# Kernel optimization log

Hardware: AMD Instinct MI355X
Metric: run time of the kernel (lower is better)

The kernel has to match this reference:

```python
import jax, jax.numpy as jnp
import numpy as np

B = 2; CIN = 64; COUT = 64; H = 192; W = 192
KH = 3; KW = 3; K = KH * KW; NC = 20
STRIDE = 1; PAD = 1; DIL = 1


def setup_inputs() -> dict:
    key = jax.random.key(0)
    ks = jax.random.split(key, 7)
    x = jax.random.normal(ks[0], (B, CIN, H, W), jnp.float32)
    input_LO = jax.random.uniform(ks[1], (B, NC, H, W), jnp.float32)
    output_LO = jax.random.uniform(ks[2], (B, NC, H, W), jnp.float32)  # HO=H, WO=W for k3 s1 p1
    weight = jax.random.normal(ks[3], (COUT, CIN, KH, KW), jnp.float32) * 0.05
    bias = jax.random.normal(ks[4], (COUT,), jnp.float32) * 0.05
    # conv_offset is zero-init in source; use small random weights so offsets are exercised
    off_w = jax.random.normal(ks[5], (2 * K, CIN, KH, KW), jnp.float32) * 0.01
    off_b = jnp.zeros((2 * K,), jnp.float32)
    return {"x": x, "input_LO": input_LO, "output_LO": output_LO,
            "weight": weight, "bias": bias, "off_w": off_w, "off_b": off_b}


def _gather(img_flat, idx):
    # img_flat: [B, C, H*W], idx: [B, N] -> [B, C, N]
    return jax.vmap(lambda im, ix: im[:, ix])(img_flat, idx)


def _bilinear(img, py, px, zero_pad):
    """Bilinear sample img [B,C,Hi,Wi] at pixel coords py/px [B,K,Ho,Wo].
    zero_pad=True -> zeros outside (deformable conv); False -> border clamp (grid_sample border)."""
    Bb, Cc, Hh, Ww = img.shape
    if not zero_pad:
        px = jnp.clip(px, 0.0, Ww - 1.0)
        py = jnp.clip(py, 0.0, Hh - 1.0)
    x0 = jnp.floor(px)
    y0 = jnp.floor(py)
    img_f = img.reshape(Bb, Cc, Hh * Ww)
    out = jnp.zeros((Bb, Cc) + px.shape[1:], img.dtype)
    for dy in (0.0, 1.0):
        for dx in (0.0, 1.0):
            yc = y0 + dy
            xc = x0 + dx
            w = (1.0 - jnp.abs(py - yc)) * (1.0 - jnp.abs(px - xc))
            if zero_pad:
                valid = (yc >= 0) & (yc <= Hh - 1) & (xc >= 0) & (xc <= Ww - 1)
                w = w * valid.astype(w.dtype)
            yi = jnp.clip(yc, 0, Hh - 1).astype(jnp.int32)
            xi = jnp.clip(xc, 0, Ww - 1).astype(jnp.int32)
            idx = (yi * Ww + xi).reshape(Bb, -1)
            g = _gather(img_f, idx).reshape((Bb, Cc) + px.shape[1:])
            out = out + g * w[:, None]
    return out


def reference(x, input_LO, output_LO, weight, bias, off_w, off_b):
    # 1) offset conv (torch chunk+cat is identity, so offset == conv_offset(x))
    offset = jax.lax.conv_general_dilated(
        x, off_w, (STRIDE, STRIDE), ((PAD, PAD), (PAD, PAD)),
        dimension_numbers=("NCHW", "OIHW", "NCHW")) + off_b[None, :, None, None]
    Bb, _, Ho, Wo = offset.shape
    off = offset.reshape(Bb, K, 2, Ho, Wo)
    off_y = off[:, :, 0]   # channel 2k   -> y offset
    off_x = off[:, :, 1]   # channel 2k+1 -> x offset
    hk = (jnp.arange(K) // KW).astype(x.dtype)[None, :, None, None]
    wk = (jnp.arange(K) % KW).astype(x.dtype)[None, :, None, None]

    # 2) mask: grid_sample label map at deformed locations (align_corners=True, border pad)
    hor = jnp.linspace(-1.0, 1.0, Wo)[None, None, None, :]
    ver = jnp.linspace(-1.0, 1.0, Ho)[None, None, :, None]
    gx = hor * STRIDE - PAD + (wk + off_x) / ((W - 1.0) / 2.0)
    gy = ver * STRIDE - PAD + (hk + off_y) / ((H - 1.0) / 2.0)
    px = (gx + 1.0) * (W - 1.0) / 2.0
    py = (gy + 1.0) * (H - 1.0) / 2.0
    samp_LO = _bilinear(input_LO, py, px, zero_pad=False)        # [B,NC,K,Ho,Wo]
    mask = jnp.einsum("bnkhw,bnhw->bkhw", samp_LO, output_LO)    # [B,K,Ho,Wo]

    # 3) modulated deformable conv (DCNv2 math, zero padding outside)
    base_y = (jnp.arange(Ho) * STRIDE - PAD).astype(x.dtype)[None, None, :, None]
    base_x = (jnp.arange(Wo) * STRIDE - PAD).astype(x.dtype)[None, None, None, :]
    py2 = base_y + hk * DIL + off_y
    px2 = base_x + wk * DIL + off_x
    samp = _bilinear(x, py2, px2, zero_pad=True)                 # [B,C,K,Ho,Wo]
    samp = samp * mask[:, None]
    out = jnp.einsum("bckhw,ock->bohw", samp, weight.reshape(COUT, CIN, K))
    return out + bias[None, :, None, None]
```

## Files before the change

kernel.cpp:

```cpp
#include <hip/hip_runtime.h>

#define Bn   2
#define CIN  64
#define COUT 64
#define Hd   192
#define Wd   192
#define HWd  (Hd*Wd)
#define Kk   9
#define NCh  20
#define NTILE 1152

typedef __attribute__((ext_vector_type(8))) short short8;
typedef __attribute__((ext_vector_type(4))) float f32x4;

static __device__ __forceinline__ ushort f2bf(float f) {
    unsigned u = __float_as_uint(f);
    u += 0x7fffu + ((u >> 16) & 1u);
    return (ushort)(u >> 16);
}
static __device__ __forceinline__ float bf2f(ushort v) {
    return __uint_as_float(((unsigned)v) << 16);
}

__global__ __launch_bounds__(256) void kT(const float* __restrict__ x,
        const float* __restrict__ inLO, const float* __restrict__ outLO,
        const float* __restrict__ w, const float* __restrict__ off_w,
        ushort* __restrict__ xtb, float* __restrict__ inLOt,
        float* __restrict__ outLOt, ushort* __restrict__ wtb,
        float* __restrict__ owt) {
    __shared__ float lds[20 * 257];
    int bid = blockIdx.x, tid = threadIdx.x;
    if (bid < 1152) {
        int b = bid / 576, p0 = (bid % 576) * 64;
        const float* src = x + b * CIN * HWd + p0;
        #pragma unroll
        for (int r = 0; r < 16; ++r) {
            int e = r * 256 + tid;
            int c = e >> 6, p = e & 63;
            lds[c * 65 + p] = src[c * HWd + p];
        }
        __syncthreads();
        ushort* dst = xtb + ((size_t)(b * HWd + p0)) * 64;
        #pragma unroll
        for (int r = 0; r < 16; ++r) {
            int e = r * 256 + tid;
            int p = e >> 6, c = e & 63;
            dst[e] = f2bf(lds[c * 65 + p]);
        }
    } else if (bid < 1728) {
        int q = bid - 1152;
        int t = q / 288; q %= 288;
        int b = q / 144, p0 = (q % 144) * 256;
        const float* src = (t == 0 ? inLO : outLO) + b * NCh * HWd + p0;
        float* dst = (t == 0 ? inLOt : outLOt) + b * NCh * HWd + p0 * NCh;
        #pragma unroll
        for (int r = 0; r < 20; ++r) {
            int e = r * 256 + tid;
            int n = e >> 8, p = e & 255;
            lds[n * 257 + p] = src[n * HWd + p];
        }
        __syncthreads();
        #pragma unroll
        for (int r = 0; r < 20; ++r) {
            int e = r * 256 + tid;
            int p = e / 20, n = e % 20;
            dst[e] = lds[n * 257 + p];
        }
    } else if (bid < 1872) {
        int f = (bid - 1728) * 256 + tid;
        int e = f & 7, lane = (f >> 3) & 63;
        int kt = (f >> 9) & 1, nt = (f >> 10) & 3, tap = f >> 12;
        int o = nt * 16 + (lane & 15);
        int c = kt * 32 + (lane >> 4) * 8 + e;
        wtb[f] = f2bf(w[(o * CIN + c) * Kk + tap]);
    } else {
        int idx = (bid - 1872) * 256 + tid;
        if (idx < 18 * 576) {
            int oc = idx % 18, ct = idx / 18;
            int c = ct / 9, tap = ct % 9;
            owt[idx] = off_w[(oc * CIN + c) * Kk + tap];
        }
    }
}

__global__ __launch_bounds__(256) void k1_offset_conv(const float* __restrict__ x,
        const float* __restrict__ owt, const float* __restrict__ off_b,
        float* __restrict__ off) {
    int tid = threadIdx.x;
    int half = blockIdx.x & 1;
    int oc0 = half * 9;
    int pix = (blockIdx.x >> 1) * 256 + tid;
    int b = pix / HWd, pp = pix % HWd;
    int jj = pp % Wd, ii = pp / Wd;
    float acc[9];
    #pragma unroll
    for (int q = 0; q < 9; ++q) acc[q] = off_b[oc0 + q];
    const float* xb = x + b * CIN * HWd;
    for (int c = 0; c < CIN; ++c) {
        const float* xc = xb + c * HWd;
        float v[9];
        #pragma unroll
        for (int dy = 0; dy < 3; ++dy) {
            int yy = ii + dy - 1;
            bool vy = (yy >= 0 && yy < Hd);
            #pragma unroll
            for (int dx = 0; dx < 3; ++dx) {
                int xx = jj + dx - 1;
                bool ok = vy && (xx >= 0) && (xx < Wd);
                int yc = min(max(yy, 0), Hd - 1);
                int xc2 = min(max(xx, 0), Wd - 1);
                float t = xc[yc * Wd + xc2];
                v[dy * 3 + dx] = ok ? t : 0.f;
            }
        }
        const float* wrow = owt + c * 9 * 18 + oc0;
        #pragma unroll
        for (int tap = 0; tap < 9; ++tap) {
            #pragma unroll
            for (int q = 0; q < 9; ++q)
                acc[q] += v[tap] * wrow[tap * 18 + q];
        }
    }
    float* op = off + b * 18 * HWd + pp;
    #pragma unroll
    for (int q = 0; q < 9; ++q) op[(oc0 + q) * HWd] = acc[q];
}

__global__ __launch_bounds__(256) void k2_mask(const float* __restrict__ inLOt,
        const float* __restrict__ outLOt, const float* __restrict__ off,
        float* __restrict__ mask) {
    int t = blockIdx.x * 256 + threadIdx.x;
    int p = t % HWd;
    int k = (t / HWd) % Kk;
    int b = t / (Kk * HWd);
    int j = p % Wd, i = p / Wd;
    float offy = off[(b * 18 + 2 * k) * HWd + p];
    float offx = off[(b * 18 + 2 * k + 1) * HWd + p];
    float py = (float)(i + (k / 3)) + offy - 95.5f;
    float px = (float)(j + (k % 3)) + offx - 95.5f;
    py = fminf(fmaxf(py, 0.f), 191.f);
    px = fminf(fmaxf(px, 0.f), 191.f);
    float y0f = floorf(py), x0f = floorf(px);
    float ly = py - y0f, lx = px - x0f;
    int y0 = (int)y0f, x0 = (int)x0f;
    int y1 = min(y0 + 1, Hd - 1), x1 = min(x0 + 1, Wd - 1);
    float w00 = (1.f - ly) * (1.f - lx);
    float w01 = (1.f - ly) * lx;
    float w10 = ly * (1.f - lx);
    float w11 = ly * lx;
    const float4* L00 = (const float4*)(inLOt + (b * HWd + y0 * Wd + x0) * NCh);
    const float4* L01 = (const float4*)(inLOt + (b * HWd + y0 * Wd + x1) * NCh);
    const float4* L10 = (const float4*)(inLOt + (b * HWd + y1 * Wd + x0) * NCh);
    const float4* L11 = (const float4*)(inLOt + (b * HWd + y1 * Wd + x1) * NCh);
    const float4* O   = (const float4*)(outLOt + (b * HWd + p) * NCh);
    float acc = 0.f;
    #pragma unroll
    for (int n = 0; n < 5; ++n) {
        float4 a = L00[n], bb = L01[n], c = L10[n], d = L11[n], o = O[n];
        acc += (w00 * a.x + w01 * bb.x + w10 * c.x + w11 * d.x) * o.x;
        acc += (w00 * a.y + w01 * bb.y + w10 * c.y + w11 * d.y) * o.y;
        acc += (w00 * a.z + w01 * bb.z + w10 * c.z + w11 * d.z) * o.z;
        acc += (w00 * a.w + w01 * bb.w + w10 * c.w + w11 * d.w) * o.w;
    }
    mask[(b * Kk + k) * HWd + p] = acc;
}

__global__ __launch_bounds__(256) void k3_part(const ushort* __restrict__ xtb,
        const float* __restrict__ off, const float* __restrict__ mask,
        const ushort* __restrict__ wtb, float* __restrict__ part) {
    __shared__ __align__(16) ushort A_lds[4 * 2 * 64 * 8];
    int tid = threadIdx.x;
    int bid = blockIdx.x;
    int h = bid >= NTILE;
    int tb = bid - (h ? NTILE : 0);
    int t0 = h ? 5 : 0, t1 = h ? 9 : 5;
    int jt = tb % 3, i = (tb / 3) % Hd, b = tb / (3 * Hd);
    int j0 = jt * 64;

    int lane = tid & 63;
    int wv_id = tid >> 6;
    int wm = wv_id >> 1;
    int wn = wv_id & 1;

    int pxo = lane & 7;
    int chunk = lane >> 3;
    int kt_s = chunk >> 2;
    int ksub = chunk & 3;
    const ushort* xb = xtb + (size_t)b * HWd * 64;

    f32x4 acc[2][2];
    #pragma unroll
    for (int mi = 0; mi < 2; ++mi)
        #pragma unroll
        for (int ni = 0; ni < 2; ++ni)
            acc[mi][ni] = (f32x4){0.f, 0.f, 0.f, 0.f};

    for (int t = t0; t < t1; ++t) {
        short8 bf[2][2];
        #pragma unroll
        for (int kt = 0; kt < 2; ++kt)
            #pragma unroll
            for (int ni = 0; ni < 2; ++ni) {
                int nt = wn * 2 + ni;
                bf[kt][ni] = *(const short8*)(wtb +
                    ((((t * 4 + nt) * 2 + kt) * 64 + lane) << 3));
            }

        #pragma unroll
        for (int r = 0; r < 2; ++r) {
            int px_loc = (wv_id << 4) + (r << 3) + pxo;
            int pix = i * Wd + j0 + px_loc;
            float offy = off[(b * 18 + 2 * t) * HWd + pix];
            float offx = off[(b * 18 + 2 * t + 1) * HWd + pix];
            float m = mask[(b * Kk + t) * HWd + pix];
            float py = (float)(i - 1 + (t / 3)) + offy;
            float px = (float)(j0 + px_loc - 1 + (t % 3)) + offx;
            float y0f = floorf(py), x0f = floorf(px);
            float ly = py - y0f, lx = px - x0f;
            int y0 = (int)y0f, x0 = (int)x0f;
            int y1 = y0 + 1, x1 = x0 + 1;
            bool vy0 = (y0 >= 0 && y0 < Hd), vy1 = (y1 >= 0 && y1 < Hd);
            bool vx0 = (x0 >= 0 && x0 < Wd), vx1 = (x1 >= 0 && x1 < Wd);
            float w00 = (vy0 && vx0) ? (1.f - ly) * (1.f - lx) * m : 0.f;
            float w01 = (vy0 && vx1) ? (1.f - ly) * lx * m : 0.f;
            float w10 = (vy1 && vx0) ? ly * (1.f - lx) * m : 0.f;
            float w11 = (vy1 && vx1) ? ly * lx * m : 0.f;
            int y0c = min(max(y0, 0), Hd - 1), y1c = min(max(y1, 0), Hd - 1);
            int x0c = min(max(x0, 0), Wd - 1), x1c = min(max(x1, 0), Wd - 1);
            const short8* g0p = (const short8*)(xb + (size_t)(y0c * Wd + x0c) * 64 + chunk * 8);
            const short8* g1p = (const short8*)(xb + (size_t)(y0c * Wd + x1c) * 64 + chunk * 8);
            const short8* g2p = (const short8*)(xb + (size_t)(y1c * Wd + x0c) * 64 + chunk * 8);
            const short8* g3p = (const short8*)(xb + (size_t)(y1c * Wd + x1c) * 64 + chunk * 8);
            short8 g0 = *g0p, g1 = *g1p, g2 = *g2p, g3 = *g3p;
            short8 pk;
            #pragma unroll
            for (int e = 0; e < 8; ++e) {
                float s = w00 * bf2f((ushort)g0[e]) + w01 * bf2f((ushort)g1[e])
                        + w10 * bf2f((ushort)g2[e]) + w11 * bf2f((ushort)g3[e]);
                pk[e] = (short)f2bf(s);
            }
            *(short8*)&A_lds[(((wv_id * 2 + kt_s) * 64 + ksub * 16 +
                               ((r << 3) + pxo)) << 3)] = pk;
        }
        __syncthreads();

        #pragma unroll
        for (int kt = 0; kt < 2; ++kt) {
            #pragma unroll
            for (int mi = 0; mi < 2; ++mi) {
                int mt2 = wm * 2 + mi;
                short8 af = *(const short8*)&A_lds[(((mt2 * 2 + kt) * 64 + lane) << 3)];
                acc[mi][0] = __builtin_amdgcn_mfma_f32_16x16x32_bf16(
                                 af, bf[kt][0], acc[mi][0], 0, 0, 0);
                acc[mi][1] = __builtin_amdgcn_mfma_f32_16x16x32_bf16(
                                 af, bf[kt][1], acc[mi][1], 0, 0, 0);
            }
        }
        __syncthreads();
    }

    float* pb = part + ((size_t)(h * NTILE + tb) << 12);
    int colo = lane & 15;
    int rb = (lane >> 4) * 4;
    #pragma unroll
    for (int ni = 0; ni < 2; ++ni) {
        int o = wn * 32 + ni * 16 + colo;
        #pragma unroll
        for (int mi = 0; mi < 2; ++mi) {
            int p0 = wm * 32 + mi * 16 + rb;
            float4 r;
            r.x = acc[mi][ni][0];
            r.y = acc[mi][ni][1];
            r.z = acc[mi][ni][2];
            r.w = acc[mi][ni][3];
            *(float4*)(pb + o * 64 + p0) = r;
        }
    }
}

__global__ __launch_bounds__(256) void k4_reduce(const float* __restrict__ part,
        const float* __restrict__ bias, float* __restrict__ out) {
    int e4 = blockIdx.x * 256 + threadIdx.x;
    int tile = e4 >> 10;
    int wi = e4 & 1023;
    int o = wi >> 4;
    int p0 = (wi & 15) << 2;
    const float4* pp = (const float4*)part;
    float4 a = pp[e4];
    float4 c = pp[e4 + NTILE * 1024];
    float bv = bias[o];
    int jt = tile % 3, i = (tile / 3) % Hd, b = tile / (3 * Hd);
    float4 r;
    r.x = a.x + c.x + bv;
    r.y = a.y + c.y + bv;
    r.z = a.z + c.z + bv;
    r.w = a.w + c.w + bv;
    *(float4*)(out + ((size_t)(b * COUT + o) * HWd) + i * Wd + jt * 64 + p0) = r;
}

extern "C" void kernel_launch(void* const* d_in, const int* in_sizes, int n_in,
                              void* d_out, int out_size, void* d_ws, size_t ws_size,
                              hipStream_t stream) {
    const float* x      = (const float*)d_in[0];
    const float* inLO   = (const float*)d_in[1];
    const float* outLO  = (const float*)d_in[2];
    const float* weight = (const float*)d_in[3];
    const float* bias   = (const float*)d_in[4];
    const float* off_w  = (const float*)d_in[5];
    const float* off_b  = (const float*)d_in[6];
    float* out = (float*)d_out;

    float*  off    = (float*)d_ws;
    float*  mask   = off    + Bn * 18 * HWd;
    ushort* wtb    = (ushort*)(mask + Bn * Kk * HWd);
    float*  owt    = (float*)(mask + Bn * Kk * HWd) + Kk * CIN * COUT;
    ushort* xtb    = (ushort*)(owt + 576 * 18);
    float*  inLOt  = (float*)(xtb + (size_t)Bn * HWd * CIN);
    float*  outLOt = inLOt  + (size_t)Bn * HWd * NCh;
    float*  part   = outLOt + (size_t)Bn * HWd * NCh;

    kT<<<1913, 256, 0, stream>>>(x, inLO, outLO, weight, off_w,
                                 xtb, inLOt, outLOt, wtb, owt);
    k1_offset_conv<<<576, 256, 0, stream>>>(x, owt, off_b, off);
    k2_mask<<<2592, 256, 0, stream>>>(inLOt, outLOt, off, mask);
    k3_part<<<2 * NTILE, 256, 0, stream>>>(xtb, off, mask, wtb, part);
    k4_reduce<<<4608, 256, 0, stream>>>(part, bias, out);
}
```

Measured before the change: 209.2 us.

## Compute offset conv with bf16 MFMA and store label maps as padded bf16

The scalar fp32 offset convolution is replaced by an implicit-GEMM kernel that reads the channel-last bf16 copy of x and accumulates with 16x16x32 bf16 MFMA instructions. Offset weights are pre-packed into the MFMA B-fragment layout, with output channels padded from 18 to 32. The input/output label maps are now transposed to bf16 with 20 channels padded to 24, so the mask kernel issues 16-byte loads and moves less data. The cost is lower precision in the offsets and the mask, and offsets feed the bilinear sample positions, so small rounding errors can shift sampling.

```diff
diff --git a/kernel.cpp b/kernel.cpp
--- a/kernel.cpp
+++ b/kernel.cpp
@@ -8,6 +8,7 @@
 #define HWd  (Hd*Wd)
 #define Kk   9
 #define NCh  20
+#define NCP  24
 #define NTILE 1152
 
 typedef __attribute__((ext_vector_type(8))) short short8;
@@ -25,9 +26,9 @@
 __global__ __launch_bounds__(256) void kT(const float* __restrict__ x,
         const float* __restrict__ inLO, const float* __restrict__ outLO,
         const float* __restrict__ w, const float* __restrict__ off_w,
-        ushort* __restrict__ xtb, float* __restrict__ inLOt,
-        float* __restrict__ outLOt, ushort* __restrict__ wtb,
-        float* __restrict__ owt) {
+        ushort* __restrict__ xtb, ushort* __restrict__ inLOb,
+        ushort* __restrict__ outLOb, ushort* __restrict__ wtb,
+        ushort* __restrict__ owtb) {
     __shared__ float lds[20 * 257];
     int bid = blockIdx.x, tid = threadIdx.x;
     if (bid < 1152) {
@@ -52,7 +53,7 @@
         int t = q / 288; q %= 288;
         int b = q / 144, p0 = (q % 144) * 256;
         const float* src = (t == 0 ? inLO : outLO) + b * NCh * HWd + p0;
-        float* dst = (t == 0 ? inLOt : outLOt) + b * NCh * HWd + p0 * NCh;
+        ushort* dst = (t == 0 ? inLOb : outLOb) + ((size_t)(b * HWd + p0)) * NCP;
         #pragma unroll
         for (int r = 0; r < 20; ++r) {
             int e = r * 256 + tid;
@@ -61,10 +62,10 @@
         }
         __syncthreads();
         #pragma unroll
-        for (int r = 0; r < 20; ++r) {
+        for (int r = 0; r < 24; ++r) {
             int e = r * 256 + tid;
-            int p = e / 20, n = e % 20;
-            dst[e] = lds[n * 257 + p];
+            int p = e / NCP, n = e - p * NCP;
+            dst[e] = (n < NCh) ? f2bf(lds[n * 257 + p]) : (ushort)0;
         }
     } else if (bid < 1872) {
         int f = (bid - 1728) * 256 + tid;
@@ -74,60 +75,72 @@
         int c = kt * 32 + (lane >> 4) * 8 + e;
         wtb[f] = f2bf(w[(o * CIN + c) * Kk + tap]);
     } else {
-        int idx = (bid - 1872) * 256 + tid;
-        if (idx < 18 * 576) {
-            int oc = idx % 18, ct = idx / 18;
-            int c = ct / 9, tap = ct % 9;
-            owt[idx] = off_w[(oc * CIN + c) * Kk + tap];
-        }
-    }
-}
-
-__global__ __launch_bounds__(256) void k1_offset_conv(const float* __restrict__ x,
-        const float* __restrict__ owt, const float* __restrict__ off_b,
+        int f = (bid - 1872) * 256 + tid;
+        if (f < 18432) {
+            int e = f & 7, lane = (f >> 3) & 63;
+            int kt = (f >> 9) & 1, nt = (f >> 10) & 1, tap = f >> 11;
+            int oc = nt * 16 + (lane & 15);
+            int c = kt * 32 + (lane >> 4) * 8 + e;
+            owtb[f] = (oc < 18) ? f2bf(off_w[(oc * CIN + c) * Kk + tap]) : (ushort)0;
+        }
+    }
+}
+
+__global__ __launch_bounds__(256) void k1_gemm(const ushort* __restrict__ xtb,
+        const ushort* __restrict__ owtb, const float* __restrict__ off_b,
         float* __restrict__ off) {
-    int tid = threadIdx.x;
-    int half = blockIdx.x & 1;
-    int oc0 = half * 9;
-    int pix = (blockIdx.x >> 1) * 256 + tid;
-    int b = pix / HWd, pp = pix % HWd;
-    int jj = pp % Wd, ii = pp / Wd;
-    float acc[9];
-    #pragma unroll
-    for (int q = 0; q < 9; ++q) acc[q] = off_b[oc0 + q];
-    const float* xb = x + b * CIN * HWd;
-    for (int c = 0; c < CIN; ++c) {
-        const float* xc = xb + c * HWd;
-        float v[9];
-        #pragma unroll
-        for (int dy = 0; dy < 3; ++dy) {
-            int yy = ii + dy - 1;
-            bool vy = (yy >= 0 && yy < Hd);
-            #pragma unroll
-            for (int dx = 0; dx < 3; ++dx) {
-                int xx = jj + dx - 1;
-                bool ok = vy && (xx >= 0) && (xx < Wd);
-                int yc = min(max(yy, 0), Hd - 1);
-                int xc2 = min(max(xx, 0), Wd - 1);
-                float t = xc[yc * Wd + xc2];
-                v[dy * 3 + dx] = ok ? t : 0.f;
-            }
-        }
-        const float* wrow = owt + c * 9 * 18 + oc0;
-        #pragma unroll
-        for (int tap = 0; tap < 9; ++tap) {
-            #pragma unroll
-            for (int q = 0; q < 9; ++q)
-                acc[q] += v[tap] * wrow[tap * 18 + q];
-        }
-    }
-    float* op = off + b * 18 * HWd + pp;
-    #pragma unroll
-    for (int q = 0; q < 9; ++q) op[(oc0 + q) * HWd] = acc[q];
-}
-
-__global__ __launch_bounds__(256) void k2_mask(const float* __restrict__ inLOt,
-        const float* __restrict__ outLOt, const float* __restrict__ off,
+    int tid = threadIdx.x, bid = blockIdx.x;
+    int jt = bid % 3, i = (bid / 3) % Hd, b = bid / (3 * Hd);
+    int j0 = jt * 64;
+    int lane = tid & 63, wv = tid >> 6;
+    int m = lane & 15;
+    int ch8 = lane >> 4;
+    int j = j0 + wv * 16 + m;
+    const ushort* xb = xtb + (size_t)b * HWd * 64;
+
+    float bv0 = off_b[m];
+    float bv1 = (m < 2) ? off_b[16 + m] : 0.f;
+    f32x4 acc0 = (f32x4){bv0, bv0, bv0, bv0};
+    f32x4 acc1 = (f32x4){bv1, bv1, bv1, bv1};
+    short8 zero8 = {0, 0, 0, 0, 0, 0, 0, 0};
+
+    #pragma unroll
+    for (int t = 0; t < 9; ++t) {
+        int yy = i + t / 3 - 1;
+        int xx = j + t % 3 - 1;
+        bool ok = (yy >= 0) && (yy < Hd) && (xx >= 0) && (xx < Wd);
+        int yc = min(max(yy, 0), Hd - 1), xc = min(max(xx, 0), Wd - 1);
+        const ushort* rowp = xb + (size_t)(yc * Wd + xc) * 64 + ch8 * 8;
+        short8 a0 = *(const short8*)rowp;
+        short8 a1 = *(const short8*)(rowp + 32);
+        a0 = ok ? a0 : zero8;
+        a1 = ok ? a1 : zero8;
+        const ushort* wb = owtb + ((size_t)t << 11);
+        short8 b00 = *(const short8*)(wb + (lane << 3));
+        short8 b01 = *(const short8*)(wb + 512 + (lane << 3));
+        short8 b10 = *(const short8*)(wb + 1024 + (lane << 3));
+        short8 b11 = *(const short8*)(wb + 1536 + (lane << 3));
+        acc0 = __builtin_amdgcn_mfma_f32_16x16x32_bf16(a0, b00, acc0, 0, 0, 0);
+        acc0 = __builtin_amdgcn_mfma_f32_16x16x32_bf16(a1, b01, acc0, 0, 0, 0);
+        acc1 = __builtin_amdgcn_mfma_f32_16x16x32_bf16(a0, b10, acc1, 0, 0, 0);
+        acc1 = __builtin_amdgcn_mfma_f32_16x16x32_bf16(a1, b11, acc1, 0, 0, 0);
+    }
+
+    int prow = j0 + wv * 16 + (lane >> 4) * 4;
+    int oc = lane & 15;
+    float* ob = off + (size_t)b * 18 * HWd + i * Wd;
+    #pragma unroll
+    for (int r = 0; r < 4; ++r)
+        ob[oc * HWd + prow + r] = acc0[r];
+    if (oc < 2) {
+        #pragma unroll
+        for (int r = 0; r < 4; ++r)
+            ob[(16 + oc) * HWd + prow + r] = acc1[r];
+    }
+}
+
+__global__ __launch_bounds__(256) void k2_mask(const ushort* __restrict__ inLOb,
+        const ushort* __restrict__ outLOb, const float* __restrict__ off,
         float* __restrict__ mask) {
     int t = blockIdx.x * 256 + threadIdx.x;
     int p = t % HWd;
@@ -148,19 +161,21 @@
     float w01 = (1.f - ly) * lx;
     float w10 = ly * (1.f - lx);
     float w11 = ly * lx;
-    const float4* L00 = (const float4*)(inLOt + (b * HWd + y0 * Wd + x0) * NCh);
-    const float4* L01 = (const float4*)(inLOt + (b * HWd + y0 * Wd + x1) * NCh);
-    const float4* L10 = (const float4*)(inLOt + (b * HWd + y1 * Wd + x0) * NCh);
-    const float4* L11 = (const float4*)(inLOt + (b * HWd + y1 * Wd + x1) * NCh);
-    const float4* O   = (const float4*)(outLOt + (b * HWd + p) * NCh);
+    const short8* L00 = (const short8*)(inLOb + (size_t)(b * HWd + y0 * Wd + x0) * NCP);
+    const short8* L01 = (const short8*)(inLOb + (size_t)(b * HWd + y0 * Wd + x1) * NCP);
+    const short8* L10 = (const short8*)(inLOb + (size_t)(b * HWd + y1 * Wd + x0) * NCP);
+    const short8* L11 = (const short8*)(inLOb + (size_t)(b * HWd + y1 * Wd + x1) * NCP);
+    const short8* O  = (const short8*)(outLOb + (size_t)(b * HWd + p) * NCP);
     float acc = 0.f;
     #pragma unroll
-    for (int n = 0; n < 5; ++n) {
-        float4 a = L00[n], bb = L01[n], c = L10[n], d = L11[n], o = O[n];
-        acc += (w00 * a.x + w01 * bb.x + w10 * c.x + w11 * d.x) * o.x;
-        acc += (w00 * a.y + w01 * bb.y + w10 * c.y + w11 * d.y) * o.y;
-        acc += (w00 * a.z + w01 * bb.z + w10 * c.z + w11 * d.z) * o.z;
-        acc += (w00 * a.w + w01 * bb.w + w10 * c.w + w11 * d.w) * o.w;
+    for (int n3 = 0; n3 < 3; ++n3) {
+        short8 a = L00[n3], bb = L01[n3], c = L10[n3], d = L11[n3], o = O[n3];
+        #pragma unroll
+        for (int e = 0; e < 8; ++e) {
+            float s = w00 * bf2f((ushort)a[e]) + w01 * bf2f((ushort)bb[e])
+                    + w10 * bf2f((ushort)c[e]) + w11 * bf2f((ushort)d[e]);
+            acc += s * bf2f((ushort)o[e]);
+        }
     }
     mask[(b * Kk + k) * HWd + p] = acc;
 }
@@ -311,18 +326,18 @@
     float* out = (float*)d_out;
 
     float*  off    = (float*)d_ws;
-    float*  mask   = off    + Bn * 18 * HWd;
+    float*  mask   = off   + Bn * 18 * HWd;
     ushort* wtb    = (ushort*)(mask + Bn * Kk * HWd);
-    float*  owt    = (float*)(mask + Bn * Kk * HWd) + Kk * CIN * COUT;
-    ushort* xtb    = (ushort*)(owt + 576 * 18);
-    float*  inLOt  = (float*)(xtb + (size_t)Bn * HWd * CIN);
-    float*  outLOt = inLOt  + (size_t)Bn * HWd * NCh;
-    float*  part   = outLOt + (size_t)Bn * HWd * NCh;
-
-    kT<<<1913, 256, 0, stream>>>(x, inLO, outLO, weight, off_w,
-                                 xtb, inLOt, outLOt, wtb, owt);
-    k1_offset_conv<<<576, 256, 0, stream>>>(x, owt, off_b, off);
-    k2_mask<<<2592, 256, 0, stream>>>(inLOt, outLOt, off, mask);
+    ushort* owtb   = wtb + 36864;
+    ushort* xtb    = owtb + 18432;
+    ushort* inLOb  = xtb + (size_t)Bn * HWd * CIN;
+    ushort* outLOb = inLOb + (size_t)Bn * HWd * NCP;
+    float*  part   = (float*)(outLOb + (size_t)Bn * HWd * NCP);
+
+    kT<<<1944, 256, 0, stream>>>(x, inLO, outLO, weight, off_w,
+                                 xtb, inLOb, outLOb, wtb, owtb);
+    k1_gemm<<<NTILE, 256, 0, stream>>>(xtb, owtb, off_b, off);
+    k2_mask<<<2592, 256, 0, stream>>>(inLOb, outLOb, off, mask);
     k3_part<<<2 * NTILE, 256, 0, stream>>>(xtb, off, mask, wtb, part);
     k4_reduce<<<4608, 256, 0, stream>>>(part, bias, out);
 }
```

New measurement: 174.6 us. -16.6%, faster.
